# Kernel tuning notes

Hardware: AMD Instinct MI355X
Metric: run time of the kernel (lower is better)

## Reference

```python
import jax, jax.numpy as jnp
import numpy as np

MAX_WAVELENGTH = 10000
BIG_NEG = -2.3819763e38


def _apply_rope(x, positions):
    """RoPE: positions [B,L] applied to x [B,L,H,D]."""
    d = x.shape[-1]
    freq_exponents = (2.0 / d) * jnp.arange(d // 2, dtype=jnp.float32)
    timescale = MAX_WAVELENGTH ** freq_exponents  # [D/2]
    radians = positions[..., None].astype(jnp.float32) / timescale  # [B,L,D/2]
    radians = radians[..., None, :]  # [B,L,1,D/2]
    sin, cos = jnp.sin(radians), jnp.cos(radians)
    x1, x2 = jnp.split(x, 2, axis=-1)
    return jnp.concatenate([x1 * cos - x2 * sin, x2 * cos + x1 * sin], axis=-1)


def setup_inputs() -> dict:
    key = jax.random.key(0)
    B, S, D, N, K, H = 2, 2048, 2048, 8, 1, 256  # batch, seq, features, q heads, kv heads, head_dim
    k1, k2, k3, k4 = jax.random.split(key, 4)
    x = jax.random.normal(k1, (B, S, D), dtype=jnp.float32)
    positions = jnp.broadcast_to(jnp.arange(S, dtype=jnp.int32), (B, S))
    attn_mask = jnp.tril(jnp.ones((S, S), dtype=bool))[None, None].repeat(B, axis=0)  # causal [B,1,S,S]
    q_w = jax.random.normal(k2, (N, D, H), dtype=jnp.float32) * (D ** -0.5)      # lecun_normal in_axis=-2
    kv_w = jax.random.normal(k3, (2, K, D, H), dtype=jnp.float32) * (D ** -0.5)
    out_w = jax.random.normal(k4, (N, H, D), dtype=jnp.float32) * (H ** -0.5)
    return {"x": x, "positions": positions, "attn_mask": attn_mask,
            "q_w": q_w, "kv_w": kv_w, "out_w": out_w}


def reference(x, positions, attn_mask, q_w, kv_w, out_w):
    B, T, D = x.shape
    N, _, H = q_w.shape
    K = kv_w.shape[1]
    G = N // K
    dtype = x.dtype

    q = jnp.einsum('btd,ndh->btnh', x, q_w)          # [B,T,N,H]
    kv = jnp.einsum('bsd,ckdh->cbskh', x, kv_w)      # [2,B,S,K,H]
    k, v = kv[0], kv[1]

    q = _apply_rope(q, positions) * (H ** -0.5)
    k = _apply_rope(k, positions)

    # prefill path: cache_size == S, so cache == k, v; idx = S
    qg = q.reshape(B, T, K, G, H)
    logits = jnp.einsum('btkgh,bskh->bkgts', qg, k,
                        preferred_element_type=jnp.float32)  # [B,K,G,T,S] fp32
    masked = jnp.where(attn_mask[:, :, None, :, :], logits, BIG_NEG)
    probs = jax.nn.softmax(masked, axis=-1).astype(dtype)
    enc = jnp.einsum('bkgts,bskh->btkgh', probs, v).reshape(B, T, N, H)
    out = jnp.einsum('btnh,nhd->btd', enc, out_w)
    return out
```

## Files before the change

kernel.cpp:

```cpp
#include <hip/hip_runtime.h>
#include <hip/hip_bf16.h>
#include <stdint.h>

#define BB 2
#define SS 2048
#define DD 2048
#define NHEAD 8
#define HH 256

typedef __bf16 bf16_t;
typedef __bf16 bf16x8 __attribute__((ext_vector_type(8)));
typedef __bf16 bf16x4v __attribute__((ext_vector_type(4)));
typedef __bf16 bf16x2v __attribute__((ext_vector_type(2)));
typedef float f32x4 __attribute__((ext_vector_type(4)));
typedef float f32x16 __attribute__((ext_vector_type(16)));
typedef unsigned int u32;

__device__ static inline void gload_lds16(const void* g, void* l) {
  __builtin_amdgcn_global_load_lds(
      (__attribute__((address_space(1))) void*)(g),
      (__attribute__((address_space(3))) void*)(l), 16, 0, 0);
}

__device__ static inline u32 pk2(float a, float b) {
  bf16x2v t = {(bf16_t)a, (bf16_t)b};
  return __builtin_bit_cast(u32, t);
}

__device__ static inline void transpose_body(const float* in, bf16_t* out, int R, int C,
                                             int bx, int by, int z, float* tile ) {
  in  += (size_t)z * R * C;
  out += (size_t)z * R * C;
  int tx = threadIdx.x & 31, ty = threadIdx.x >> 5;
#pragma unroll
  for (int k = 0; k < 4; ++k) {
    int r = by * 32 + ty + k * 8, c = bx * 32 + tx;
    tile[(ty + k * 8) * 33 + tx] = in[(size_t)r * C + c];
  }
  __syncthreads();
#pragma unroll
  for (int k = 0; k < 4; ++k) {
    int c = bx * 32 + ty + k * 8, r = by * 32 + tx;
    out[(size_t)c * R + r] = (bf16_t)tile[tx * 33 + ty + k * 8];
  }
}

__global__ void prep_kernel(const float* __restrict__ x, bf16_t* __restrict__ xb,
                            const float* __restrict__ qw, const float* __restrict__ kvw,
                            const float* __restrict__ outw, bf16_t* __restrict__ qkvwbt,
                            bf16_t* __restrict__ outwbt) {
  __shared__ float tile[32 * 33];
  int bid = blockIdx.x;
  if (bid < 8192) {
    size_t i = ((size_t)bid * 256 + threadIdx.x) * 4;
    float4 v = *(const float4*)(x + i);
    bf16x4v o = {(bf16_t)v.x, (bf16_t)v.y, (bf16_t)v.z, (bf16_t)v.w};
    *(bf16x4v*)(xb + i) = o;
  } else if (bid < 8192 + 4096) {
    int b2 = bid - 8192;
    transpose_body(qw, qkvwbt, 2048, 256, b2 & 7, (b2 >> 3) & 63, b2 >> 9, tile);
  } else if (bid < 8192 + 4096 + 1024) {
    int b2 = bid - (8192 + 4096);
    transpose_body(kvw, qkvwbt + (size_t)2048 * 2048, 2048, 256, b2 & 7, (b2 >> 3) & 63,
                   b2 >> 9, tile);
  } else {
    int b2 = bid - (8192 + 4096 + 1024);
    transpose_body(outw, outwbt, 2048, 2048, b2 & 63, b2 >> 6, 0, tile);
  }
}

template <int OUT_F32>
__global__ __launch_bounds__(256) void gemm2b(const bf16_t* __restrict__ A,
                                              const bf16_t* __restrict__ BT,
                                              void* __restrict__ C,
                                              int M, int Nc, int Kd) {
  __shared__ __attribute__((aligned(16))) char LDS[81920];
  char* Abuf = LDS;
  char* Bbuf = LDS + 49152;
  const int ntiles = Nc >> 7;
  int nwg = gridDim.x;
  int bid = ((nwg & 7) == 0) ? ((blockIdx.x & 7) * (nwg >> 3) + (blockIdx.x >> 3))
                             : blockIdx.x;
  int mt = bid / ntiles, ntb = bid % ntiles;
  int t = threadIdx.x, lane = t & 63, w = t >> 6;
  int wm = w >> 1, wn = w & 1;
  int l15 = lane & 15, lg = lane >> 4;
  int srow = t >> 3;
  int scolb = ((t & 7) * 16) ^ ((srow & 7) << 4);
  const bf16_t* Asrc = A + (size_t)(mt * 128 + srow) * Kd + (scolb >> 1);
  const bf16_t* Bsrc = BT + (size_t)(ntb * 128 + srow) * Kd + (scolb >> 1);
  const int nkt = Kd >> 6;
  f32x4 acc[4][4] = {};

#define STAGE_A(kt_)                                                  \
  {                                                                   \
    char* d_ = Abuf + ((kt_) % 3) * 16384 + t * 16;                   \
    const bf16_t* s_ = Asrc + (kt_)*64;                               \
    gload_lds16(s_, d_);                                              \
    gload_lds16(s_ + (size_t)32 * Kd, d_ + 4096);                     \
    gload_lds16(s_ + (size_t)64 * Kd, d_ + 8192);                     \
    gload_lds16(s_ + (size_t)96 * Kd, d_ + 12288);                    \
  }
#define STAGE_B(kt_)                                                  \
  {                                                                   \
    char* d_ = Bbuf + ((kt_)&1) * 16384 + t * 16;                     \
    const bf16_t* s_ = Bsrc + (kt_)*64;                               \
    gload_lds16(s_, d_);                                              \
    gload_lds16(s_ + (size_t)32 * Kd, d_ + 4096);                     \
    gload_lds16(s_ + (size_t)64 * Kd, d_ + 8192);                     \
    gload_lds16(s_ + (size_t)96 * Kd, d_ + 12288);                    \
  }

  STAGE_A(0);
  STAGE_B(0);
  STAGE_A(1);
  asm volatile("s_waitcnt vmcnt(4)" ::: "memory");
  __builtin_amdgcn_s_barrier();
  asm volatile("" ::: "memory");
  for (int kt = 0; kt < nkt; ++kt) {
    if (kt + 1 < nkt) STAGE_B(kt + 1);
    if (kt + 2 < nkt) STAGE_A(kt + 2);
    const char* Ab = Abuf + (kt % 3) * 16384;
    const char* Bb = Bbuf + (kt & 1) * 16384;
    int swz = (l15 & 7) << 4;
#pragma unroll
    for (int ks = 0; ks < 2; ++ks) {
      bf16x8 af[4], bfr[4];
#pragma unroll
      for (int i = 0; i < 4; ++i)
        af[i] = *(const bf16x8*)(Ab + (wm * 64 + i * 16 + l15) * 128 +
                                 ((ks * 64 + lg * 16) ^ swz));
#pragma unroll
      for (int j = 0; j < 4; ++j)
        bfr[j] = *(const bf16x8*)(Bb + (wn * 64 + j * 16 + l15) * 128 +
                                  ((ks * 64 + lg * 16) ^ swz));
      __builtin_amdgcn_s_setprio(1);
#pragma unroll
      for (int i = 0; i < 4; ++i)
#pragma unroll
        for (int j = 0; j < 4; ++j)
          acc[i][j] = __builtin_amdgcn_mfma_f32_16x16x32_bf16(af[i], bfr[j], acc[i][j], 0, 0, 0);
      __builtin_amdgcn_s_setprio(0);
    }
    if (kt + 1 < nkt) {
      if (kt + 2 < nkt) {
        asm volatile("s_waitcnt vmcnt(4)" ::: "memory");
      } else {
        asm volatile("s_waitcnt vmcnt(0)" ::: "memory");
      }
      __builtin_amdgcn_s_barrier();
      asm volatile("" ::: "memory");
    }
  }
#undef STAGE_A
#undef STAGE_B
#pragma unroll
  for (int i = 0; i < 4; ++i)
#pragma unroll
    for (int j = 0; j < 4; ++j) {
      int row = mt * 128 + wm * 64 + i * 16 + lg * 4;
      int col = ntb * 128 + wn * 64 + j * 16 + l15;
#pragma unroll
      for (int v = 0; v < 4; ++v) {
        if (OUT_F32)
          ((float*)C)[(size_t)(row + v) * Nc + col] = acc[i][j][v];
        else
          ((bf16_t*)C)[(size_t)(row + v) * Nc + col] = (bf16_t)acc[i][j][v];
      }
    }
}

__global__ void ropevt_kernel(bf16_t* __restrict__ qkv, const int* __restrict__ positions,
                              bf16_t* __restrict__ vt) {
  if (blockIdx.x < 2304) {
    int idx = blockIdx.x * 256 + threadIdx.x;
    const int QP = 4096 * 8 * 16;
    int i0, row;
    bf16_t* p1;
    float scl;
    if (idx < QP) {
      i0 = (idx & 15) * 8;
      int nh = (idx >> 4) & 7;
      row = idx >> 7;
      p1 = qkv + (size_t)row * 2560 + nh * 256 + i0;
      scl = 0.0625f;
    } else {
      int kk = idx - QP;
      i0 = (kk & 15) * 8;
      row = kk >> 4;
      p1 = qkv + (size_t)row * 2560 + 2048 + i0;
      scl = 1.0f;
    }
    float pos = (float)positions[row];
    bf16x8 v1 = *(const bf16x8*)p1;
    bf16x8 v2 = *(const bf16x8*)(p1 + 128);
    bf16x8 o1, o2;
#pragma unroll
    for (int j = 0; j < 8; ++j) {
      float ang = pos * __expf(-(float)(i0 + j) * (9.2103403719761836f / 128.f));
      float s = __sinf(ang), c = __cosf(ang);
      float x1 = (float)v1[j], x2 = (float)v2[j];
      o1[j] = (bf16_t)((x1 * c - x2 * s) * scl);
      o2[j] = (bf16_t)((x2 * c + x1 * s) * scl);
    }
    *(bf16x8*)p1 = o1;
    *(bf16x8*)(p1 + 128) = o2;
  } else {
    __shared__ bf16_t tile[32][34];
    int b2 = blockIdx.x - 2304;
    int bx = b2 & 63, by = (b2 >> 6) & 7, b = b2 >> 9;
    int tx = threadIdx.x & 31, ty = threadIdx.x >> 5;
#pragma unroll
    for (int k = 0; k < 4; ++k) {
      int s = bx * 32 + ty + k * 8, h = by * 32 + tx;
      tile[ty + k * 8][tx] = qkv[((size_t)(b * SS + s)) * 2560 + 2304 + h];
    }
    __syncthreads();
#pragma unroll
    for (int k = 0; k < 4; ++k) {
      int h = by * 32 + ty + k * 8, s = bx * 32 + tx;
      vt[((size_t)(b * HH + h)) * 2048 + s] = tile[tx][ty + k * 8];
    }
  }
}

__global__ __launch_bounds__(512)
void flash_kernel(const bf16_t* __restrict__ qkv, const bf16_t* __restrict__ vtg,
                  bf16_t* __restrict__ enc, u32* __restrict__ ctr) {
  __shared__ __attribute__((aligned(16))) char LDSRAW[149504];
  char* Kl = LDSRAW;
  char* Vl = LDSRAW + 65536;
  char* Pl = LDSRAW + 131072;
  float* lsumL = (float*)(LDSRAW + 147456);
  u32* slot = (u32*)(LDSRAW + 148992);
  int t = threadIdx.x, lane = t & 63, w = t >> 6;
  int l31 = lane & 31, h5 = lane >> 5;
  bool isQK = (w < 4);
  int wq = isQK ? (w & 1) : ((w - 4) & 1);
  int sh = (w >> 1) & 1;
  int hh = ((w - 4) >> 1) & 1;
  int rk0 = t >> 5;
  int cbk = ((t & 31) * 16) ^ ((rk0 & 15) << 4);
  int rv0 = t >> 3;
  int cbv = ((t & 7) * 16) ^ ((rv0 & 7) << 4);

  for (;;) {
    if (t == 0) *slot = atomicAdd(ctr, 1);
    __syncthreads();
    u32 ti = *slot;
    if (ti >= 512u) break;
    int qt = 31 - (int)(ti >> 4);
    int b = (int)(ti >> 3) & 1, n = (int)ti & 7;
    const bf16_t* kbase = qkv + (size_t)(b * SS) * 2560 + 2048;
    int qmin = qt * 64 + wq * 32;
    int q_g = qmin + l31;
    bf16x8 qf[16];
    if (isQK) {
      const bf16_t* qrow = qkv + ((size_t)(b * SS + q_g)) * 2560 + n * 256 + h5 * 8;
#pragma unroll
      for (int i = 0; i < 16; ++i) qf[i] = *(const bf16x8*)(qrow + i * 16);
    }
    f32x16 accO[4] = {};
    float l_r = 0.f;
#pragma unroll
    for (int r = 0; r < 4; ++r)
      gload_lds16(kbase + (size_t)(rk0 + 16 * r) * 2560 + (cbk >> 1), Kl + t * 16 + r * 8192);
    __syncthreads();
    for (int kt = 0; kt <= qt + 1; ++kt) {
      int cur = kt & 1, prv = cur ^ 1;
      if (kt <= qt) {
#pragma unroll
        for (int r = 0; r < 4; ++r)
          gload_lds16(vtg + ((size_t)(b * HH + rv0 + 64 * r)) * 2048 + kt * 64 + (cbv >> 1),
                      Vl + cur * 32768 + t * 16 + r * 8192);
      }
      if (kt < qt) {
#pragma unroll
        for (int r = 0; r < 4; ++r)
          gload_lds16(kbase + (size_t)((kt + 1) * 64 + rk0 + 16 * r) * 2560 + (cbk >> 1),
                      Kl + prv * 32768 + t * 16 + r * 8192);
      }
      bool act = isQK && (kt <= qt) && (kt * 64 + sh * 32 <= qmin + 31);
      bool pact = (!isQK) && (kt >= 1);
      if (act) {
        const char* Kc = Kl + cur * 32768;
        int krow = sh * 32 + l31;
        int kswz = (l31 & 15) << 4;
        f32x16 scA = {}, scB = {};
        __builtin_amdgcn_s_setprio(1);
#pragma unroll
        for (int i = 0; i < 8; ++i) {
          bf16x8 kfa = *(const bf16x8*)(Kc + krow * 512 + (((2 * i) * 32 + h5 * 16) ^ kswz));
          bf16x8 kfb = *(const bf16x8*)(Kc + krow * 512 + (((2 * i + 1) * 32 + h5 * 16) ^ kswz));
          scA = __builtin_amdgcn_mfma_f32_32x32x16_bf16(kfa, qf[2 * i], scA, 0, 0, 0);
          scB = __builtin_amdgcn_mfma_f32_32x32x16_bf16(kfb, qf[2 * i + 1], scB, 0, 0, 0);
        }
        __builtin_amdgcn_s_setprio(0);
        f32x16 sc = scA + scB;
        int smin = kt * 64 + sh * 32;
        if (smin + 31 > qmin) {
#pragma unroll
          for (int r = 0; r < 16; ++r) {
            int s_g = smin + ((r & 3) + 8 * (r >> 2) + 4 * h5);
            if (s_g > q_g) sc[r] = -1e30f;
          }
        }
        float rs = 0.f;
#pragma unroll
        for (int r = 0; r < 16; ++r) {
          float p = __expf(sc[r] - 8.f);
          sc[r] = p;
          rs += p;
        }
        rs += __shfl_xor(rs, 32);
        l_r += rs;
        u32 u0 = pk2(sc[0], sc[1]),  u1 = pk2(sc[2], sc[3]);
        u32 u2 = pk2(sc[4], sc[5]),  u3 = pk2(sc[6], sc[7]);
        u32 u4 = pk2(sc[8], sc[9]),  u5 = pk2(sc[10], sc[11]);
        u32 u6 = pk2(sc[12], sc[13]), u7 = pk2(sc[14], sc[15]);
        u32 x0 = __shfl_xor(u0, 32), x1 = __shfl_xor(u1, 32);
        u32 x2 = __shfl_xor(u2, 32), x3 = __shfl_xor(u3, 32);
        u32 x4 = __shfl_xor(u4, 32), x5 = __shfl_xor(u5, 32);
        u32 x6 = __shfl_xor(u6, 32), x7 = __shfl_xor(u7, 32);
        union { u32 wd[4]; bf16x8 v; } f0, f1;
        f0.wd[0] = h5 ? x2 : u0;  f0.wd[1] = h5 ? x3 : u1;
        f0.wd[2] = h5 ? u2 : x0;  f0.wd[3] = h5 ? u3 : x1;
        f1.wd[0] = h5 ? x6 : u4;  f1.wd[1] = h5 ? x7 : u5;
        f1.wd[2] = h5 ? u6 : x4;  f1.wd[3] = h5 ? u7 : x5;
        char* Pw = Pl + cur * 8192 + wq * 4096;
        int pswz = (l31 & 7) << 4;
        *(bf16x8*)(Pw + l31 * 128 + ((sh * 64 + h5 * 16) ^ pswz)) = f0.v;
        *(bf16x8*)(Pw + l31 * 128 + ((sh * 64 + 32 + h5 * 16) ^ pswz)) = f1.v;
      }
      if (pact) {
        const char* Pw = Pl + prv * 8192 + wq * 4096;
        const char* Vc = Vl + prv * 32768;
        int pswz = (l31 & 7) << 4;
        int jmax = ((kt - 1 < qt) || wq == 1) ? 4 : 2;
        __builtin_amdgcn_s_setprio(1);
        for (int j = 0; j < jmax; ++j) {
          bf16x8 pf = *(const bf16x8*)(Pw + l31 * 128 + ((j * 32 + h5 * 16) ^ pswz));
#pragma unroll
          for (int ht = 0; ht < 4; ++ht) {
            int vrow = hh * 128 + ht * 32 + l31;
            bf16x8 vf = *(const bf16x8*)(Vc + vrow * 128 + ((j * 32 + h5 * 16) ^ pswz));
            accO[ht] = __builtin_amdgcn_mfma_f32_32x32x16_bf16(pf, vf, accO[ht], 0, 0, 0);
          }
        }
        __builtin_amdgcn_s_setprio(0);
      }
      __syncthreads();
    }
    if (isQK && h5 == 0) lsumL[sh * 64 + wq * 32 + l31] = l_r;
    __syncthreads();
    if (!isQK) {
      float lt = lsumL[wq * 32 + l31] + lsumL[64 + wq * 32 + l31];
      float rinv = 1.f / lt;
      float riv[16];
#pragma unroll
      for (int r = 0; r < 16; ++r) riv[r] = __shfl(rinv, (r & 3) + 8 * (r >> 2) + 4 * h5);
#pragma unroll
      for (int ht = 0; ht < 4; ++ht)
#pragma unroll
        for (int r = 0; r < 16; ++r) {
          int ql = (r & 3) + 8 * (r >> 2) + 4 * h5;
          enc[((size_t)(b * SS + qmin + ql)) * 2048 + n * 256 + hh * 128 + ht * 32 + l31] =
              (bf16_t)(accO[ht][r] * riv[r]);
        }
    }
    __syncthreads();
  }
}

extern "C" void kernel_launch(void* const* d_in, const int* in_sizes, int n_in,
                              void* d_out, int out_size, void* d_ws, size_t ws_size,
                              hipStream_t stream) {
  const float* x = (const float*)d_in[0];
  const int* positions = (const int*)d_in[1];
  const float* qw = (const float*)d_in[3];
  const float* kvw = (const float*)d_in[4];
  const float* outw = (const float*)d_in[5];

  char* ws = (char*)d_ws;
  if (ws_size < (size_t)75497472) return;
  bf16_t* xb      = (bf16_t*)(ws);
  bf16_t* qkvwbt  = (bf16_t*)(ws + 16777216);
  bf16_t* outwbt  = (bf16_t*)(ws + 27262976);
  bf16_t* qkvb    = (bf16_t*)(ws + 35651584);
  bf16_t* vtg     = (bf16_t*)(ws + 56623104);
  bf16_t* encb    = (bf16_t*)(ws + 58720256);
  u32* ctr        = (u32*)(ws);

  prep_kernel<<<17408, 256, 0, stream>>>(x, xb, qw, kvw, outw, qkvwbt, outwbt);
  gemm2b<0><<<640, 256, 0, stream>>>(xb, qkvwbt, qkvb, 4096, 2560, 2048);
  ropevt_kernel<<<3328, 256, 0, stream>>>(qkvb, positions, vtg);
  hipMemsetAsync(ctr, 0, 4, stream);
  flash_kernel<<<256, 512, 0, stream>>>(qkvb, vtg, encb, ctr);
  gemm2b<1><<<512, 256, 0, stream>>>(encb, outwbt, d_out, 4096, 2048, 2048);
}
```

Baseline: 179.9 us.

## Add K=32 triple-buffered GEMM variant with smaller LDS for QKV projection

Adds a new GEMM kernel that stages 32-wide K slices through a three-deep LDS ring of 48 KB, replacing the previous 80 KB-LDS kernel for the QKV projection only. The smaller LDS footprint could let two workgroups share a CU and hide latency through occupancy. The cost is twice as many barriers and K iterations, with less MFMA work between each sync. The output projection keeps using the old kernel.

Result: slower. 184.4 us (+2.5%).

```diff
diff --git a/kernel.cpp b/kernel.cpp
--- a/kernel.cpp
+++ b/kernel.cpp
@@ -67,6 +67,92 @@
     int b2 = bid - (8192 + 4096 + 1024);
     transpose_body(outw, outwbt, 2048, 2048, b2 & 63, b2 >> 6, 0, tile);
   }
+}
+
+template <int OUT_F32>
+__global__ __launch_bounds__(256) void gemm32(const bf16_t* __restrict__ A,
+                                              const bf16_t* __restrict__ BT,
+                                              void* __restrict__ C,
+                                              int M, int Nc, int Kd) {
+  __shared__ __attribute__((aligned(16))) char LDS[49152];
+  char* Abuf = LDS;
+  char* Bbuf = LDS + 24576;
+  const int ntiles = Nc >> 7;
+  int nwg = gridDim.x;
+  int bid = ((nwg & 7) == 0) ? ((blockIdx.x & 7) * (nwg >> 3) + (blockIdx.x >> 3))
+                             : blockIdx.x;
+  int mt = bid / ntiles, ntb = bid % ntiles;
+  int t = threadIdx.x, lane = t & 63, w = t >> 6;
+  int wm = w >> 1, wn = w & 1;
+  int l15 = lane & 15, lg = lane >> 4;
+  int srow = t >> 2;
+  int scolb = (((t & 3) ^ ((t >> 3) & 3)) << 4);
+  const bf16_t* Asrc = A + (size_t)(mt * 128 + srow) * Kd + (scolb >> 1);
+  const bf16_t* Bsrc = BT + (size_t)(ntb * 128 + srow) * Kd + (scolb >> 1);
+  const int nkt = Kd >> 5;
+  f32x4 acc[4][4] = {};
+
+#define STAGE32(kt_)                                                  \
+  {                                                                   \
+    char* da_ = Abuf + ((kt_) % 3) * 8192 + t * 16;                   \
+    char* db_ = Bbuf + ((kt_) % 3) * 8192 + t * 16;                   \
+    const bf16_t* sa_ = Asrc + (kt_)*32;                              \
+    const bf16_t* sb_ = Bsrc + (kt_)*32;                              \
+    gload_lds16(sa_, da_);                                            \
+    gload_lds16(sa_ + (size_t)64 * Kd, da_ + 4096);                   \
+    gload_lds16(sb_, db_);                                            \
+    gload_lds16(sb_ + (size_t)64 * Kd, db_ + 4096);                   \
+  }
+
+  STAGE32(0);
+  STAGE32(1);
+  asm volatile("s_waitcnt vmcnt(4)" ::: "memory");
+  __builtin_amdgcn_s_barrier();
+  asm volatile("" ::: "memory");
+  for (int kt = 0; kt < nkt; ++kt) {
+    if (kt + 2 < nkt) STAGE32(kt + 2);
+    const char* Ab = Abuf + (kt % 3) * 8192;
+    const char* Bb = Bbuf + (kt % 3) * 8192;
+    int col = (lg ^ ((l15 >> 1) & 3)) << 4;
+    bf16x8 af[4], bfr[4];
+#pragma unroll
+    for (int i = 0; i < 4; ++i)
+      af[i] = *(const bf16x8*)(Ab + (wm * 64 + i * 16 + l15) * 64 + col);
+#pragma unroll
+    for (int j = 0; j < 4; ++j)
+      bfr[j] = *(const bf16x8*)(Bb + (wn * 64 + j * 16 + l15) * 64 + col);
+    __builtin_amdgcn_s_setprio(1);
+#pragma unroll
+    for (int i = 0; i < 4; ++i)
+#pragma unroll
+      for (int j = 0; j < 4; ++j)
+        acc[i][j] = __builtin_amdgcn_mfma_f32_16x16x32_bf16(af[i], bfr[j], acc[i][j], 0, 0, 0);
+    __builtin_amdgcn_s_setprio(0);
+    if (kt + 1 < nkt) {
+      if (kt + 2 < nkt) {
+        asm volatile("s_waitcnt vmcnt(4)" ::: "memory");
+      } else {
+        asm volatile("s_waitcnt vmcnt(0)" ::: "memory");
+      }
+      __builtin_amdgcn_s_barrier();
+      asm volatile("" ::: "memory");
+    }
+  }
+#undef STAGE32
+#pragma unroll
+  for (int i = 0; i < 4; ++i)
+#pragma unroll
+    for (int j = 0; j < 4; ++j) {
+      int row = mt * 128 + wm * 64 + i * 16 + lg * 4;
+      int col = ntb * 128 + wn * 64 + j * 16 + l15;
+#pragma unroll
+      for (int v = 0; v < 4; ++v) {
+        if (OUT_F32)
+          ((float*)C)[(size_t)(row + v) * Nc + col] = acc[i][j][v];
+        else
+          ((bf16_t*)C)[(size_t)(row + v) * Nc + col] = (bf16_t)acc[i][j][v];
+      }
+    }
 }
 
 template <int OUT_F32>
@@ -392,7 +478,7 @@
   u32* ctr        = (u32*)(ws);
 
   prep_kernel<<<17408, 256, 0, stream>>>(x, xb, qw, kvw, outw, qkvwbt, outwbt);
-  gemm2b<0><<<640, 256, 0, stream>>>(xb, qkvwbt, qkvb, 4096, 2560, 2048);
+  gemm32<0><<<640, 256, 0, stream>>>(xb, qkvwbt, qkvb, 4096, 2560, 2048);
   ropevt_kernel<<<3328, 256, 0, stream>>>(qkvb, positions, vtg);
   hipMemsetAsync(ctr, 0, 4, stream);
   flash_kernel<<<256, 512, 0, stream>>>(qkvb, vtg, encb, ctr);
```
